# Kernel optimization log

Hardware: AMD Instinct MI355X
Metric: run time of the kernel (lower is better)

## Reference

```python
import jax, jax.numpy as jnp
from jax import lax
import numpy as np

D = 128      # embedding_dim == GRU input_size == hidden_size
B, S, L = 256, 32, 32  # users, slates per user, slate length


def setup_inputs() -> dict:
    key = jax.random.key(0)
    ks = jax.random.split(key, 8)
    sc = 1.0 / np.sqrt(D)  # PyTorch GRU/Linear init scale
    return {
        "item_embs": jax.random.normal(ks[0], (B, S, L, D), jnp.float32),
        "user_embs": jax.random.normal(ks[1], (B, S, D), jnp.float32),
        "W_ih": jax.random.normal(ks[2], (3 * D, D), jnp.float32) * sc,
        "W_hh": jax.random.normal(ks[3], (3 * D, D), jnp.float32) * sc,
        "b_ih": jax.random.normal(ks[4], (3 * D,), jnp.float32) * sc,
        "b_hh": jax.random.normal(ks[5], (3 * D,), jnp.float32) * sc,
        "W_out": jax.random.normal(ks[6], (1, D), jnp.float32) * sc,
        "b_out": jax.random.normal(ks[7], (1,), jnp.float32) * sc,
    }


def reference(item_embs, user_embs, W_ih, W_hh, b_ih, b_hh, W_out, b_out):
    b, s, l, d = item_embs.shape
    x = item_embs.reshape(b * s, l, d)          # [N, L, D]
    h0 = user_embs.reshape(b * s, d)            # [N, D] initial hidden per slate

    # Precompute input-side gate projections for all timesteps (one big GEMM).
    gx = jnp.einsum('nld,gd->nlg', x, W_ih) + b_ih  # [N, L, 3D], PyTorch gate order r,z,n

    def step(h, gx_t):
        gh = h @ W_hh.T + b_hh                   # [N, 3D]
        xr, xz, xn = jnp.split(gx_t, 3, axis=-1)
        hr, hz, hn = jnp.split(gh, 3, axis=-1)
        r = jax.nn.sigmoid(xr + hr)
        z = jax.nn.sigmoid(xz + hz)
        n = jnp.tanh(xn + r * hn)
        h_new = (1.0 - z) * n + z * h
        return h_new, h_new

    _, hs = lax.scan(step, h0, jnp.swapaxes(gx, 0, 1))  # hs: [L, N, D]
    rnn_out = jnp.swapaxes(hs, 0, 1)             # [N, L, D]
    out = rnn_out @ W_out.T + b_out              # [N, L, 1]
    return out.reshape(b, s, l)
```

## Files before the change

kernel.cpp:

```cpp
#include <hip/hip_runtime.h>
#include <math.h>

#define DD   128
#define LL   32
#define MS   16
#define NT   512
#define NSEQ 8192
#define XHP  264
#define OLP  36

typedef short bf16x8 __attribute__((ext_vector_type(8)));
typedef float f32x4  __attribute__((ext_vector_type(4)));

__device__ __forceinline__ unsigned short f2bf(float f) {
    unsigned u = __float_as_uint(f);
    u += 0x7fffu + ((u >> 16) & 1u);
    return (unsigned short)(u >> 16);
}

#if __has_builtin(__builtin_amdgcn_cvt_pk_bf16_f32)
typedef __bf16 bf16x2_t __attribute__((ext_vector_type(2)));
__device__ __forceinline__ unsigned pack2(float a, float b) {
    union { bf16x2_t v; unsigned u; } c;
    c.v = __builtin_amdgcn_cvt_pk_bf16_f32(a, b);
    return c.u;
}
#else
__device__ __forceinline__ unsigned pack2(float a, float b) {
    return (unsigned)f2bf(a) | ((unsigned)f2bf(b) << 16);
}
#endif

__device__ __forceinline__ void pack8(float4 a, float4 b, unsigned short* dst) {
    union { unsigned u[4]; bf16x8 v; } pk;
    pk.u[0] = pack2(a.x, a.y); pk.u[1] = pack2(a.z, a.w);
    pk.u[2] = pack2(b.x, b.y); pk.u[3] = pack2(b.z, b.w);
    *(bf16x8*)dst = pk.v;
}

__device__ __forceinline__ float fast_rcp(float x) {
    return __builtin_amdgcn_rcpf(x);
}

__global__ void prep_weights(const float* __restrict__ Wih,
                             const float* __restrict__ Whh,
                             unsigned short* __restrict__ Wfrag) {
    int idx = blockIdx.x * blockDim.x + threadIdx.x;
    int j    = idx & 7;
    int lane = (idx >> 3) & 63;
    int kk   = (idx >> 9) & 7;
    int ct   = idx >> 12;
    int n = lane & 15, q = lane >> 4;
    float v = 0.f;
    if (ct < 16) {
        int g = ct * 16 + n;
        int k = kk * 32 + q * 8 + j;
        v = (k < 128) ? Wih[g * 128 + k] : Whh[g * 128 + (k - 128)];
    } else if (ct < 24) {
        if (kk < 4) {
            int g = 256 + (ct - 16) * 16 + n;
            int k = kk * 32 + q * 8 + j;
            v = Wih[g * 128 + k];
        }
    } else {
        if (kk >= 4) {
            int g = 256 + (ct - 24) * 16 + n;
            int k = kk * 32 + q * 8 + j - 128;
            v = Whh[g * 128 + k];
        }
    }
    Wfrag[idx] = f2bf(v);
}

__global__ __launch_bounds__(NT, 2) void gru_mfma(
    const float* __restrict__ x,
    const float* __restrict__ h0,
    const unsigned short* __restrict__ Wfrag,
    const float* __restrict__ b_ih,
    const float* __restrict__ b_hh,
    const float* __restrict__ w_out,
    const float* __restrict__ b_out,
    float* __restrict__ out)
{
    __shared__ __align__(16) unsigned short xh[2][MS][XHP];
    __shared__ __align__(16) unsigned short wofl[4 * 64 * 8];
    __shared__ __align__(16) float outl[MS][OLP];

    const int tid  = threadIdx.x;
    const int n0   = blockIdx.x * MS;
    const int wv   = tid >> 6;
    const int lane = tid & 63;
    const int ln   = lane & 15;
    const int q    = lane >> 4;
    const int gn   = (tid >> 4) & 15;
    const int gd8  = (tid & 15) * 8;
    const int d    = wv * 16 + ln;

    const float br  = b_ih[d]        + b_hh[d];
    const float bz  = b_ih[DD + d]   + b_hh[DD + d];
    const float bin = b_ih[2*DD + d];
    const float bhn = b_hh[2*DD + d];
    const float bo  = b_out[0];

    bf16x8 wrz0[8], wrz1[8], wxn[4], whn[4];
    {
        const bf16x8* W = (const bf16x8*)Wfrag;
        #pragma unroll
        for (int kk = 0; kk < 8; ++kk) {
            wrz0[kk] = W[((wv    ) * 8 + kk) * 64 + lane];
            wrz1[kk] = W[((wv + 8) * 8 + kk) * 64 + lane];
        }
        #pragma unroll
        for (int kk = 0; kk < 4; ++kk) {
            wxn[kk] = W[((wv + 16) * 8 + kk    ) * 64 + lane];
            whn[kk] = W[((wv + 24) * 8 + kk + 4) * 64 + lane];
        }
    }

    #pragma unroll
    for (int e = 0; e < 4; ++e) {
        int idx = tid * 4 + e;
        int j   = idx & 7;
        int l2  = (idx >> 3) & 63;
        int kk  = idx >> 9;
        int n2 = l2 & 15, q2 = l2 >> 4;
        wofl[idx] = (n2 == 0) ? f2bf(w_out[kk * 32 + q2 * 8 + j])
                              : (unsigned short)0;
    }

    float hprev[4];
    #pragma unroll
    for (int i = 0; i < 4; ++i)
        hprev[i] = h0[(size_t)(n0 + q*4 + i) * DD + d];

    const float* xbase = x + ((size_t)(n0 + gn) * LL) * DD + gd8;
    float4 xa0, xa1, xb0, xb1;
    if (tid < 256) {
        const float* hb = h0 + (size_t)(n0 + gn) * DD + gd8;
        pack8(*(const float4*)hb, *(const float4*)(hb + 4), &xh[0][gn][DD + gd8]);
        pack8(*(const float4*)xbase, *(const float4*)(xbase + 4), &xh[0][gn][gd8]);
        xa0 = *(const float4*)(xbase + 1 * DD);
        xa1 = *(const float4*)(xbase + 1 * DD + 4);
        xb0 = *(const float4*)(xbase + 2 * DD);
        xb1 = *(const float4*)(xbase + 2 * DD + 4);
    }
    __syncthreads();

#define GRU_STEP(PAR, XR0, XR1, TCUR, TREFILL)                                 \
    {                                                                          \
                       \
        if (tid < 256) {                                                       \
            pack8(XR0, XR1, &xh[(PAR) ^ 1][gn][gd8]);                          \
            XR0 = *(const float4*)(xbase + (size_t)(TREFILL) * DD);            \
            XR1 = *(const float4*)(xbase + (size_t)(TREFILL) * DD + 4);        \
        }                                                                      \
                                   \
        f32x4 c0 = {0.f,0.f,0.f,0.f}, c1 = c0, c2 = c0, c3 = c0;               \
        const unsigned short* xr0 = &xh[PAR][ln][0];                           \
        _Pragma("unroll")                                                      \
        for (int kk = 0; kk < 8; ++kk) {                                       \
            bf16x8 a0 = *(const bf16x8*)(xr0 + kk*32 + q*8);                   \
            c0 = __builtin_amdgcn_mfma_f32_16x16x32_bf16(a0, wrz0[kk], c0,0,0,0); \
            c1 = __builtin_amdgcn_mfma_f32_16x16x32_bf16(a0, wrz1[kk], c1,0,0,0); \
            if (kk < 4) c2 = __builtin_amdgcn_mfma_f32_16x16x32_bf16(a0, wxn[kk],   c2,0,0,0); \
            else        c3 = __builtin_amdgcn_mfma_f32_16x16x32_bf16(a0, whn[kk-4], c3,0,0,0); \
        }                                                                      \
                         \
        if (wv == 0 && (TCUR) > 0) {                                           \
            f32x4 c4 = {0.f,0.f,0.f,0.f};                                      \
            _Pragma("unroll")                                                  \
            for (int kk = 0; kk < 4; ++kk) {                                   \
                bf16x8 a = *(const bf16x8*)(xr0 + (kk+4)*32 + q*8);            \
                bf16x8 b = *(const bf16x8*)&wofl[(kk*64 + lane)*8];            \
                c4 = __builtin_amdgcn_mfma_f32_16x16x32_bf16(a, b, c4,0,0,0);  \
            }                                                                  \
            if (ln == 0) {                                                     \
                _Pragma("unroll")                                              \
                for (int i = 0; i < 4; ++i)                                    \
                    outl[q*4 + i][(TCUR)-1] = c4[i] + bo;                      \
            }                                                                  \
        }                                                                      \
                       \
        _Pragma("unroll")                                                      \
        for (int i = 0; i < 4; ++i) {                                          \
            const float rr = fast_rcp(1.f + __expf(-(c0[i] + br)));            \
            const float zz = fast_rcp(1.f + __expf(-(c1[i] + bz)));            \
            float aa = c2[i] + bin + rr * (c3[i] + bhn);                       \
            aa = fminf(fmaxf(aa, -20.f), 20.f);                                \
            const float ee = __expf(-2.f * aa);                                \
            const float th = (1.f - ee) * fast_rcp(1.f + ee);                  \
            const float hh = th + zz * (hprev[i] - th);                        \
            hprev[i] = hh;                                                     \
            xh[(PAR) ^ 1][q*4 + i][DD + d] = f2bf(hh);                         \
        }                                                                      \
        __syncthreads();                                                       \
    }

    for (int t = 0; t < LL; t += 2) {
        const int r0 = (t + 3 < LL) ? t + 3 : LL - 1;
        const int r1 = (t + 4 < LL) ? t + 4 : LL - 1;
        GRU_STEP(0, xa0, xa1, t,     r0)
        GRU_STEP(1, xb0, xb1, t + 1, r1)
    }
#undef GRU_STEP

    if (wv == 0) {
        f32x4 c4 = {0.f,0.f,0.f,0.f};
        const unsigned short* xr = &xh[0][ln][0];
        #pragma unroll
        for (int kk = 0; kk < 4; ++kk) {
            bf16x8 a = *(const bf16x8*)(xr + (kk+4)*32 + q*8);
            bf16x8 b = *(const bf16x8*)&wofl[(kk*64 + lane)*8];
            c4 = __builtin_amdgcn_mfma_f32_16x16x32_bf16(a, b, c4,0,0,0);
        }
        if (ln == 0) {
            #pragma unroll
            for (int i = 0; i < 4; ++i)
                outl[q*4 + i][LL-1] = c4[i] + bo;
        }
    }
    __syncthreads();

    if (tid < 128) {
        const int row = tid >> 3;
        const int t4  = (tid & 7) * 4;
        float4 v = *(const float4*)&outl[row][t4];
        *(float4*)(out + (size_t)(n0 + row) * LL + t4) = v;
    }
}

extern "C" void kernel_launch(void* const* d_in, const int* in_sizes, int n_in,
                              void* d_out, int out_size, void* d_ws, size_t ws_size,
                              hipStream_t stream) {
    const float* item  = (const float*)d_in[0];
    const float* user  = (const float*)d_in[1];
    const float* W_ih  = (const float*)d_in[2];
    const float* W_hh  = (const float*)d_in[3];
    const float* b_ih  = (const float*)d_in[4];
    const float* b_hh  = (const float*)d_in[5];
    const float* W_out = (const float*)d_in[6];
    const float* b_out = (const float*)d_in[7];
    float* out = (float*)d_out;

    unsigned short* Wfrag = (unsigned short*)d_ws;

    prep_weights<<<512, 256, 0, stream>>>(W_ih, W_hh, Wfrag);
    gru_mfma<<<NSEQ / MS, NT, 0, stream>>>(item, user, Wfrag,
                                           b_ih, b_hh, W_out, b_out, out);
}
```

Baseline: 228.4 us.

## Process two 16-sequence groups per block and interleave their MFMA and gate phases

Each block now handles 32 sequences instead of 16, split into two halves. The recurrent step for each half is staggered so that one half's matrix multiply runs alongside the other half's gate nonlinearities, with each phase ending at a barrier. This is meant to hide the serial dependency between MFMA and transcendental math, and it halves the number of blocks. The costs are twice as many barriers per timestep, more registers for two sets of accumulators, and fewer blocks, which may leave CUs underused.

```diff
diff --git a/kernel.cpp b/kernel.cpp
--- a/kernel.cpp
+++ b/kernel.cpp
@@ -3,7 +3,7 @@
 
 #define DD   128
 #define LL   32
-#define MS   16
+#define MS   32
 #define NT   512
 #define NSEQ 8192
 #define XHP  264
@@ -92,7 +92,7 @@
     const int lane = tid & 63;
     const int ln   = lane & 15;
     const int q    = lane >> 4;
-    const int gn   = (tid >> 4) & 15;
+    const int gn   = tid >> 4;
     const int gd8  = (tid & 15) * 8;
     const int d    = wv * 16 + ln;
 
@@ -128,70 +128,93 @@
                               : (unsigned short)0;
     }
 
-    float hprev[4];
+    float hprev[8];
     #pragma unroll
-    for (int i = 0; i < 4; ++i)
-        hprev[i] = h0[(size_t)(n0 + q*4 + i) * DD + d];
-
-    const float* xbase = x + ((size_t)(n0 + gn) * LL) * DD + gd8;
-    float4 xa0, xa1, xb0, xb1;
-    if (tid < 256) {
+    for (int tl = 0; tl < 2; ++tl)
+        #pragma unroll
+        for (int i = 0; i < 4; ++i)
+            hprev[tl*4+i] = h0[(size_t)(n0 + tl*16 + q*4 + i) * DD + d];
+
+    {
         const float* hb = h0 + (size_t)(n0 + gn) * DD + gd8;
         pack8(*(const float4*)hb, *(const float4*)(hb + 4), &xh[0][gn][DD + gd8]);
-        pack8(*(const float4*)xbase, *(const float4*)(xbase + 4), &xh[0][gn][gd8]);
-        xa0 = *(const float4*)(xbase + 1 * DD);
-        xa1 = *(const float4*)(xbase + 1 * DD + 4);
-        xb0 = *(const float4*)(xbase + 2 * DD);
-        xb1 = *(const float4*)(xbase + 2 * DD + 4);
-    }
+    }
+    const float* xbase = x + ((size_t)(n0 + gn) * LL) * DD + gd8;
+    pack8(*(const float4*)xbase, *(const float4*)(xbase + 4), &xh[0][gn][gd8]);
+    float4 xa0 = *(const float4*)(xbase + 1 * DD);
+    float4 xa1 = *(const float4*)(xbase + 1 * DD + 4);
+    float4 xb0 = *(const float4*)(xbase + 2 * DD);
+    float4 xb1 = *(const float4*)(xbase + 2 * DD + 4);
     __syncthreads();
 
-#define GRU_STEP(PAR, XR0, XR1, TCUR, TREFILL)                                 \
+    f32x4 c0a, c1a, c2a, c3a;
+    f32x4 c0b, c1b, c2b, c3b;
+
+#define MFMA24(XRPTR, C0, C1, C2, C3)                                          \
+    do {                                                                       \
+        C0 = (f32x4){0.f,0.f,0.f,0.f}; C1 = C0; C2 = C0; C3 = C0;              \
+        const unsigned short* xr_ = (XRPTR);                                   \
+        _Pragma("unroll")                                                      \
+        for (int kk = 0; kk < 8; ++kk) {                                       \
+            bf16x8 a_ = *(const bf16x8*)(xr_ + kk*32 + q*8);                   \
+            C0 = __builtin_amdgcn_mfma_f32_16x16x32_bf16(a_, wrz0[kk], C0,0,0,0); \
+            C1 = __builtin_amdgcn_mfma_f32_16x16x32_bf16(a_, wrz1[kk], C1,0,0,0); \
+            if (kk < 4) C2 = __builtin_amdgcn_mfma_f32_16x16x32_bf16(a_, wxn[kk],   C2,0,0,0); \
+            else        C3 = __builtin_amdgcn_mfma_f32_16x16x32_bf16(a_, whn[kk-4], C3,0,0,0); \
+        }                                                                      \
+    } while (0)
+
+#define GATE(C0, C1, C2, C3, HB, ROWB, DSTBUF)                                 \
+    do {                                                                       \
+        _Pragma("unroll")                                                      \
+        for (int i = 0; i < 4; ++i) {                                          \
+            const float rr = fast_rcp(1.f + __expf(-(C0[i] + br)));            \
+            const float zz = fast_rcp(1.f + __expf(-(C1[i] + bz)));            \
+            float aa = C2[i] + bin + rr * (C3[i] + bhn);                       \
+            aa = fminf(fmaxf(aa, -20.f), 20.f);                                \
+            const float ee = __expf(-2.f * aa);                                \
+            const float th = (1.f - ee) * fast_rcp(1.f + ee);                  \
+            const float hh = th + zz * (hprev[(HB)+i] - th);                   \
+            hprev[(HB)+i] = hh;                                                \
+            xh[DSTBUF][(ROWB) + q*4 + i][DD + d] = f2bf(hh);                   \
+        }                                                                      \
+    } while (0)
+
+#define PHASE_A(PAR, XR0, XR1, T, TR)                                          \
     {                                                                          \
-                       \
         if (tid < 256) {                                                       \
             pack8(XR0, XR1, &xh[(PAR) ^ 1][gn][gd8]);                          \
-            XR0 = *(const float4*)(xbase + (size_t)(TREFILL) * DD);            \
-            XR1 = *(const float4*)(xbase + (size_t)(TREFILL) * DD + 4);        \
-        }                                                                      \
-                                   \
-        f32x4 c0 = {0.f,0.f,0.f,0.f}, c1 = c0, c2 = c0, c3 = c0;               \
-        const unsigned short* xr0 = &xh[PAR][ln][0];                           \
-        _Pragma("unroll")                                                      \
-        for (int kk = 0; kk < 8; ++kk) {                                       \
-            bf16x8 a0 = *(const bf16x8*)(xr0 + kk*32 + q*8);                   \
-            c0 = __builtin_amdgcn_mfma_f32_16x16x32_bf16(a0, wrz0[kk], c0,0,0,0); \
-            c1 = __builtin_amdgcn_mfma_f32_16x16x32_bf16(a0, wrz1[kk], c1,0,0,0); \
-            if (kk < 4) c2 = __builtin_amdgcn_mfma_f32_16x16x32_bf16(a0, wxn[kk],   c2,0,0,0); \
-            else        c3 = __builtin_amdgcn_mfma_f32_16x16x32_bf16(a0, whn[kk-4], c3,0,0,0); \
-        }                                                                      \
-                         \
-        if (wv == 0 && (TCUR) > 0) {                                           \
+            XR0 = *(const float4*)(xbase + (size_t)(TR) * DD);                 \
+            XR1 = *(const float4*)(xbase + (size_t)(TR) * DD + 4);             \
+        }                                                                      \
+        MFMA24(&xh[PAR][ln][0], c0a, c1a, c2a, c3a);                           \
+        if ((T) > 0) GATE(c0b, c1b, c2b, c3b, 4, 16, PAR);                     \
+        __syncthreads();                                                       \
+    }
+
+#define PHASE_B(PAR, XR0, XR1, T, TR)                                          \
+    {                                                                          \
+        if (tid >= 256) {                                                      \
+            pack8(XR0, XR1, &xh[(PAR) ^ 1][gn][gd8]);                          \
+            XR0 = *(const float4*)(xbase + (size_t)(TR) * DD);                 \
+            XR1 = *(const float4*)(xbase + (size_t)(TR) * DD + 4);             \
+        }                                                                      \
+        MFMA24(&xh[PAR][16 + ln][0], c0b, c1b, c2b, c3b);                      \
+        GATE(c0a, c1a, c2a, c3a, 0, 0, (PAR) ^ 1);                             \
+        if ((T) > 0 && wv < 2) {                                               \
             f32x4 c4 = {0.f,0.f,0.f,0.f};                                      \
+            const unsigned short* xr_ = &xh[PAR][wv*16 + ln][0];               \
             _Pragma("unroll")                                                  \
             for (int kk = 0; kk < 4; ++kk) {                                   \
-                bf16x8 a = *(const bf16x8*)(xr0 + (kk+4)*32 + q*8);            \
-                bf16x8 b = *(const bf16x8*)&wofl[(kk*64 + lane)*8];            \
-                c4 = __builtin_amdgcn_mfma_f32_16x16x32_bf16(a, b, c4,0,0,0);  \
+                bf16x8 a_ = *(const bf16x8*)(xr_ + (kk+4)*32 + q*8);           \
+                bf16x8 b_ = *(const bf16x8*)&wofl[(kk*64 + lane)*8];           \
+                c4 = __builtin_amdgcn_mfma_f32_16x16x32_bf16(a_, b_, c4,0,0,0);\
             }                                                                  \
             if (ln == 0) {                                                     \
                 _Pragma("unroll")                                              \
                 for (int i = 0; i < 4; ++i)                                    \
-                    outl[q*4 + i][(TCUR)-1] = c4[i] + bo;                      \
+                    outl[wv*16 + q*4 + i][(T)-1] = c4[i] + bo;                 \
             }                                                                  \
-        }                                                                      \
-                       \
-        _Pragma("unroll")                                                      \
-        for (int i = 0; i < 4; ++i) {                                          \
-            const float rr = fast_rcp(1.f + __expf(-(c0[i] + br)));            \
-            const float zz = fast_rcp(1.f + __expf(-(c1[i] + bz)));            \
-            float aa = c2[i] + bin + rr * (c3[i] + bhn);                       \
-            aa = fminf(fmaxf(aa, -20.f), 20.f);                                \
-            const float ee = __expf(-2.f * aa);                                \
-            const float th = (1.f - ee) * fast_rcp(1.f + ee);                  \
-            const float hh = th + zz * (hprev[i] - th);                        \
-            hprev[i] = hh;                                                     \
-            xh[(PAR) ^ 1][q*4 + i][DD + d] = f2bf(hh);                         \
         }                                                                      \
         __syncthreads();                                                       \
     }
@@ -199,14 +222,20 @@
     for (int t = 0; t < LL; t += 2) {
         const int r0 = (t + 3 < LL) ? t + 3 : LL - 1;
         const int r1 = (t + 4 < LL) ? t + 4 : LL - 1;
-        GRU_STEP(0, xa0, xa1, t,     r0)
-        GRU_STEP(1, xb0, xb1, t + 1, r1)
-    }
-#undef GRU_STEP
-
-    if (wv == 0) {
+        PHASE_A(0, xa0, xa1, t,     r0)
+        PHASE_B(0, xa0, xa1, t,     r0)
+        PHASE_A(1, xb0, xb1, t + 1, r1)
+        PHASE_B(1, xb0, xb1, t + 1, r1)
+    }
+#undef PHASE_A
+#undef PHASE_B
+
+    GATE(c0b, c1b, c2b, c3b, 4, 16, 0);
+    __syncthreads();
+
+    if (wv < 2) {
         f32x4 c4 = {0.f,0.f,0.f,0.f};
-        const unsigned short* xr = &xh[0][ln][0];
+        const unsigned short* xr = &xh[0][wv*16 + ln][0];
         #pragma unroll
         for (int kk = 0; kk < 4; ++kk) {
             bf16x8 a = *(const bf16x8*)(xr + (kk+4)*32 + q*8);
@@ -216,17 +245,19 @@
         if (ln == 0) {
             #pragma unroll
             for (int i = 0; i < 4; ++i)
-                outl[q*4 + i][LL-1] = c4[i] + bo;
+                outl[wv*16 + q*4 + i][LL-1] = c4[i] + bo;
         }
     }
     __syncthreads();
 
-    if (tid < 128) {
+    if (tid < 256) {
         const int row = tid >> 3;
         const int t4  = (tid & 7) * 4;
         float4 v = *(const float4*)&outl[row][t4];
         *(float4*)(out + (size_t)(n0 + row) * LL + t4) = v;
     }
+#undef MFMA24
+#undef GATE
 }
 
 extern "C" void kernel_launch(void* const* d_in, const int* in_sizes, int n_in,
```

New measurement: 224.4 us. About the same (-1.7%).
